# Kernel optimization log

Measured on AMD Instinct MI355X. Metric: run time of the kernel, lower is better.

The kernel has to match this reference:

```python
import jax, jax.numpy as jnp
import numpy as np

B, N, D, H, E, ED = 32, 256, 1024, 16, 512, 256
HD = D // H
NEG = float(np.finfo(np.float32).min)


def setup_inputs() -> dict:
    key = jax.random.key(0)
    ks = iter(jax.random.split(key, 16))
    def nrm(shape, fan_in):
        return jax.random.normal(next(ks), shape, jnp.float32) / np.sqrt(fan_in)
    return {
        "x": jax.random.normal(next(ks), (B, N, D), jnp.float32),
        "node_masks": jnp.ones((B, N), jnp.float32),
        "relation_edges": jax.random.randint(next(ks), (B, E, 2), 0, N, jnp.int64),
        "relation_masks": jnp.ones((B, E), jnp.float32),
        "relation_embeddings": jax.random.normal(next(ks), (B, E, ED), jnp.float32),
        "ln_g": jnp.ones((D,), jnp.float32), "ln_b": jnp.zeros((D,), jnp.float32),
        "Wq": nrm((D, D), D), "bq": jnp.zeros((D,), jnp.float32),
        "Wk": nrm((D, D), D), "bk": jnp.zeros((D,), jnp.float32),
        "Wv": nrm((D, D), D), "bv": jnp.zeros((D,), jnp.float32),
        "We": nrm((ED, H), ED), "be": jnp.zeros((H,), jnp.float32),
        "Wo": nrm((D, D), D), "bo": jnp.zeros((D,), jnp.float32),
        "ff_g": jnp.ones((D,), jnp.float32), "ff_b": jnp.zeros((D,), jnp.float32),
        "W1": nrm((D, 4 * D), D), "b1": jnp.zeros((4 * D,), jnp.float32),
        "W2": nrm((4 * D, D), 4 * D), "b2": jnp.zeros((D,), jnp.float32),
    }


def _ln(x, g, b):
    m = jnp.mean(x, axis=-1, keepdims=True)
    v = jnp.mean((x - m) ** 2, axis=-1, keepdims=True)
    return (x - m) / jnp.sqrt(v + 1e-5) * g + b


def reference(x, node_masks, relation_edges, relation_masks, relation_embeddings,
              ln_g, ln_b, Wq, bq, Wk, bk, Wv, bv, We, be, Wo, bo,
              ff_g, ff_b, W1, b1, W2, b2):
    residual = x
    xn = _ln(x, ln_g, ln_b)
    # [B,N,D] -> [B,H,N,HD]
    def split_heads(t):
        return t.reshape(B, N, H, HD).transpose(0, 2, 1, 3)
    q = split_heads(xn @ Wq + bq)
    k = split_heads(xn @ Wk + bk)
    v = split_heads(xn @ Wv + bv)
    attn = jnp.einsum('bhqd,bhkd->bhqk', q, k) / np.sqrt(HD)

    nb = node_masks.astype(bool)
    pair_mask = nb[:, None, :, None] & nb[:, None, None, :]  # [B,1,N,N]

    # --- scatter edge list into dense adjacency + per-head bias ---
    src = jnp.clip(relation_edges[..., 0], 0, N - 1)  # [B,E]
    dst = jnp.clip(relation_edges[..., 1], 0, N - 1)
    valid = relation_masks.astype(bool)
    # route invalid edges to a padding row/col N, sliced off afterwards
    src_w = jnp.where(valid, src, N)
    dst_w = jnp.where(valid, dst, N)
    b_idx = jnp.broadcast_to(jnp.arange(B)[:, None], (B, E))

    Np = N + 1
    adj = jnp.broadcast_to(jnp.eye(Np, dtype=bool), (B, Np, Np))
    adj = adj.at[b_idx, src_w, dst_w].set(True).at[b_idx, dst_w, src_w].set(True)
    rel_adj = adj[:, :N, :N][:, None]  # [B,1,N,N]

    eb = relation_embeddings @ We + be  # [B,E,H]
    bias = jnp.zeros((B, Np, Np, H), x.dtype)
    bias = bias.at[b_idx, src_w, dst_w].set(eb).at[b_idx, dst_w, src_w].set(eb)
    rel_bias = bias[:, :N, :N, :].transpose(0, 3, 1, 2)  # [B,H,N,N]

    attn = attn + rel_bias
    pair_mask = pair_mask & rel_adj
    attn = jnp.where(pair_mask, attn, NEG)
    attn = jax.nn.softmax(attn, axis=-1)
    attn = jnp.nan_to_num(attn)

    out = jnp.einsum('bhqk,bhkd->bhqd', attn, v).transpose(0, 2, 1, 3).reshape(B, N, D)
    x = residual + (out @ Wo + bo)
    h = _ln(x, ff_g, ff_b)
    h = jax.nn.silu(h @ W1 + b1) @ W2 + b2
    x = x + h
    return x * node_masks[..., None]
```

## Files before the change

kernel.cpp:

```cpp
#include <hip/hip_runtime.h>
#include <math.h>

#define B_  32
#define N_  256
#define D_  1024
#define H_  16
#define E_  512
#define ED_ 256
#define HD_ 64
#define QS_ 3072
#define NEG_ (-3.4028234663852886e38f)

typedef __attribute__((ext_vector_type(8))) short short8;
typedef __attribute__((ext_vector_type(4))) float f32x4;
typedef __attribute__((ext_vector_type(16))) float f32x16;
typedef unsigned short ushort_t;
typedef unsigned int uint_t;

union U16x8 { uint4 u4; ushort_t s[8]; };

static __device__ __forceinline__ ushort_t f2bf(float f) {
    uint_t u = __builtin_bit_cast(uint_t, f);
    u = (u + 0x7fff + ((u >> 16) & 1)) >> 16;
    return (ushort_t)u;
}

static __device__ __forceinline__ void gload_lds16(const void* g, void* l) {
    __builtin_amdgcn_global_load_lds(
        (const __attribute__((address_space(1))) unsigned int*)g,
        (__attribute__((address_space(3))) unsigned int*)l, 16, 0, 0);
}

__global__ __launch_bounds__(256) void ln_bf16_kernel(const float* __restrict__ x,
                                                      const float* __restrict__ g,
                                                      const float* __restrict__ b,
                                                      ushort_t* __restrict__ out) {
    int row = blockIdx.x;
    const float* xr = x + (size_t)row * D_;
    ushort_t* yr = out + (size_t)row * D_;
    __shared__ float red[256];
    int t = threadIdx.x;
    float vals[4];
    float s = 0.f;
#pragma unroll
    for (int i = 0; i < 4; ++i) { vals[i] = xr[t + i * 256]; s += vals[i]; }
    red[t] = s; __syncthreads();
    for (int off = 128; off > 0; off >>= 1) { if (t < off) red[t] += red[t + off]; __syncthreads(); }
    float mean = red[0] * (1.f / D_);
    __syncthreads();
    float vs = 0.f;
#pragma unroll
    for (int i = 0; i < 4; ++i) { float d = vals[i] - mean; vs += d * d; }
    red[t] = vs; __syncthreads();
    for (int off = 128; off > 0; off >>= 1) { if (t < off) red[t] += red[t + off]; __syncthreads(); }
    float rstd = 1.f / sqrtf(red[0] * (1.f / D_) + 1e-5f);
#pragma unroll
    for (int i = 0; i < 4; ++i) {
        int c = t + i * 256;
        yr[c] = f2bf((vals[i] - mean) * rstd * g[c] + b[c]);
    }
}

__global__ __launch_bounds__(256) void prep_kernel(
    const float* __restrict__ Wq, const float* __restrict__ Wk,
    const float* __restrict__ Wv, const float* __restrict__ Wo,
    const float* __restrict__ W1, const float* __restrict__ W2,
    const float* __restrict__ bq, const float* __restrict__ bk,
    const float* __restrict__ bv,
    ushort_t* __restrict__ qkvT, ushort_t* __restrict__ WoT,
    ushort_t* __restrict__ W1T, ushort_t* __restrict__ W2T,
    float* __restrict__ cb)
{
    int id = blockIdx.x;
    if (id >= 12288) {
        int i = (id - 12288) * 256 + threadIdx.x;
        cb[i] = (i < 1024) ? bq[i] : ((i < 2048) ? bk[i - 1024] : bv[i - 2048]);
        return;
    }
    const float* in; ushort_t* outp; int K, N, tid;
    if (id < 4096) {
        int wsel = id >> 10; tid = id & 1023; K = D_; N = D_;
        in   = (wsel == 0) ? Wq : (wsel == 1) ? Wk : (wsel == 2) ? Wv : Wo;
        outp = (wsel == 0) ? qkvT : (wsel == 1) ? qkvT + 1024 * 1024
             : (wsel == 2) ? qkvT + 2 * 1024 * 1024 : WoT;
    } else if (id < 8192) { tid = id - 4096; K = D_; N = 4 * D_; in = W1; outp = W1T; }
    else                  { tid = id - 8192; K = 4 * D_; N = D_; in = W2; outp = W2T; }
    int tilesX = N >> 5;
    int n0 = (tid % tilesX) * 32, k0 = (tid / tilesX) * 32;

    __shared__ float tile[32][33];
    int tx = threadIdx.x & 31, ty = threadIdx.x >> 5;
#pragma unroll
    for (int r = 0; r < 4; ++r)
        tile[ty + r * 8][tx] = in[(size_t)(k0 + ty + r * 8) * N + n0 + tx];
    __syncthreads();
#pragma unroll
    for (int r = 0; r < 4; ++r)
        outp[(size_t)(n0 + ty + r * 8) * K + k0 + tx] = f2bf(tile[tx][ty + r * 8]);
}

__global__ __launch_bounds__(256) void eb_kernel(const float* __restrict__ re,
                                                 const float* __restrict__ We,
                                                 const float* __restrict__ be,
                                                 float* __restrict__ eb) {
    __shared__ float rs[16 * 256];
    __shared__ float wl[256 * 16];
    int t = threadIdx.x;
    int be0 = blockIdx.x * 16;
#pragma unroll
    for (int i = 0; i < 16; ++i) wl[t + i * 256] = We[t + i * 256];
#pragma unroll
    for (int i = 0; i < 16; ++i) rs[t + i * 256] = re[(size_t)be0 * 256 + t + i * 256];
    __syncthreads();
    int el = t >> 4, h = t & 15;
    float s = be[h];
#pragma unroll 8
    for (int i = 0; i < 256; ++i) s += rs[el * 256 + i] * wl[i * 16 + h];
    eb[(size_t)(be0 + el) * 16 + h] = s;
}

__global__ void scatter_kernel(const int* __restrict__ edges, const float* __restrict__ emask,
                               int* __restrict__ prio) {
    int idx = blockIdx.x * blockDim.x + threadIdx.x;
    if (idx >= B_ * E_) return;
    if (emask[idx] == 0.f) return;
    int b = idx / E_, e = idx % E_;
    int s = edges[2 * idx], d = edges[2 * idx + 1];
    s = min(max(s, 0), N_ - 1);
    d = min(max(d, 0), N_ - 1);
    int* base = prio + (size_t)b * N_ * N_;
    atomicMax(&base[s * N_ + d], e);
    atomicMax(&base[d * N_ + s], e + E_);
}

template<int MODE>
__global__ __launch_bounds__(256) void gemm_bf16(
    const ushort_t* __restrict__ A, const ushort_t* __restrict__ BT,
    const float* __restrict__ bias, const float* __restrict__ res,
    const float* __restrict__ nm, void* __restrict__ Cout,
    int M, int N, int K)
{
    __shared__ ushort_t As[128 * 32];
    __shared__ ushort_t Bs[128 * 32];
    int t = threadIdx.x;
    int lane = t & 63;
    int l31 = lane & 31, lh = lane >> 5;
    int w = t >> 6;
    int wr = (w >> 1) * 64, wc = (w & 1) * 64;

    int bid = blockIdx.x;
    int xcd = bid & 7;
    int lid = bid >> 3;
    int st  = lid >> 5;
    int ls  = lid & 31;
    int brow = xcd * 8 + (ls >> 2);
    int bcol = st * 4 + (ls & 3);
    int row0 = brow * 128, col0 = bcol * 128;

    const ushort_t* Ag = A + (size_t)row0 * K;
    const ushort_t* Bg = BT + (size_t)col0 * K;
    int r0 = t >> 2;
    int sl = t & 3;
    int sc = (sl ^ ((r0 >> 1) & 3)) * 8;

    f32x16 acc[2][2];
#pragma unroll
    for (int i = 0; i < 2; ++i)
#pragma unroll
        for (int j = 0; j < 2; ++j)
#pragma unroll
            for (int r = 0; r < 16; ++r) acc[i][j][r] = 0.f;

    for (int k0 = 0; k0 < K; k0 += 32) {
        gload_lds16(Ag + (size_t)r0 * K + k0 + sc, (char*)As + t * 16);
        gload_lds16(Ag + (size_t)(64 + r0) * K + k0 + sc, (char*)As + 4096 + t * 16);
        gload_lds16(Bg + (size_t)r0 * K + k0 + sc, (char*)Bs + t * 16);
        gload_lds16(Bg + (size_t)(64 + r0) * K + k0 + sc, (char*)Bs + 4096 + t * 16);
        __syncthreads();
#pragma unroll
        for (int ks = 0; ks < 2; ++ks) {
            short8 af[2], bf[2];
#pragma unroll
            for (int it = 0; it < 2; ++it) {
                int m = wr + it * 32 + l31;
                int x = ((ks * 2 + lh) ^ ((m >> 1) & 3)) * 8;
                af[it] = *(const short8*)(const void*)(As + m * 32 + x);
            }
#pragma unroll
            for (int jt = 0; jt < 2; ++jt) {
                int n = wc + jt * 32 + l31;
                int x = ((ks * 2 + lh) ^ ((n >> 1) & 3)) * 8;
                bf[jt] = *(const short8*)(const void*)(Bs + n * 32 + x);
            }
#pragma unroll
            for (int it = 0; it < 2; ++it)
#pragma unroll
                for (int jt = 0; jt < 2; ++jt)
                    acc[it][jt] = __builtin_amdgcn_mfma_f32_32x32x16_bf16(af[it], bf[jt], acc[it][jt], 0, 0, 0);
        }
        __syncthreads();
    }

#pragma unroll
    for (int it = 0; it < 2; ++it) {
#pragma unroll
        for (int jt = 0; jt < 2; ++jt) {
            int col = col0 + wc + jt * 32 + l31;
            float bcol_b = bias[col];
#pragma unroll
            for (int reg = 0; reg < 16; ++reg) {
                int row = row0 + wr + it * 32 + (reg & 3) + 8 * (reg >> 2) + 4 * lh;
                float v = acc[it][jt][reg] + bcol_b;
                if (MODE == 0) {
                    ((ushort_t*)Cout)[(size_t)row * N + col] = f2bf(v);
                } else if (MODE == 1) {
                    ((float*)Cout)[(size_t)row * N + col] = v + res[(size_t)row * N + col];
                } else if (MODE == 2) {
                    v = v / (1.f + __expf(-v));
                    ((ushort_t*)Cout)[(size_t)row * N + col] = f2bf(v);
                } else {
                    v = (v + res[(size_t)row * N + col]) * nm[row];
                    ((float*)Cout)[(size_t)row * N + col] = v;
                }
            }
        }
    }
}

__global__ __launch_bounds__(256, 2) void attn_mfma_kernel(
    const ushort_t* __restrict__ qkv, const int* __restrict__ prio,
    const float* __restrict__ eb, const float* __restrict__ nm,
    ushort_t* __restrict__ out)
{
    int xb = blockIdx.x;
    int bid = (xb & 7) * 256 + (xb >> 3);
    int h = bid & 15, qt = (bid >> 4) & 3, b = bid >> 6;
    int t = threadIdx.x;

    __shared__ ushort_t Ks[256 * 72];
    __shared__ ushort_t Vt[64 * 264];

    int lane = t & 63, c = lane & 15, quad = lane >> 4;
    int w = t >> 6;
    int qbase = qt * 64 + w * 16 + quad * 4;

    int pr[16][4];
    const int* prp = prio + ((size_t)(b * N_ + qbase)) * N_ + c;
#pragma unroll
    for (int j = 0; j < 16; ++j)
#pragma unroll
        for (int r = 0; r < 4; ++r)
            pr[j][r] = prp[(size_t)r * N_ + j * 16];

    float nmq[4];
#pragma unroll
    for (int r = 0; r < 4; ++r) nmq[r] = nm[b * N_ + qbase + r];
    float nmk[16];
#pragma unroll
    for (int j = 0; j < 16; ++j) nmk[j] = nm[b * N_ + j * 16 + c];

    const ushort_t* qg = qkv + ((size_t)(b * N_ + qt * 64 + w * 16 + c)) * QS_ + h * HD_;
    short8 aq0 = *(const short8*)(const void*)(qg + quad * 8);
    short8 aq1 = *(const short8*)(const void*)(qg + 32 + quad * 8);

    int lr = t >> 3, lc = (t & 7) * 8;
    const ushort_t* kg = qkv + ((size_t)(b * N_)) * QS_ + 1024 + h * HD_;
#pragma unroll
    for (int r = 0; r < 256; r += 32)
        *(uint4*)&Ks[(lr + r) * 72 + lc] = *(const uint4*)&kg[(size_t)(lr + r) * QS_ + lc];
    const ushort_t* vg = qkv + ((size_t)(b * N_)) * QS_ + 2048 + h * HD_;
#pragma unroll
    for (int r = 0; r < 256; r += 32) {
        U16x8 uu; uu.u4 = *(const uint4*)&vg[(size_t)(lr + r) * QS_ + lc];
#pragma unroll
        for (int i = 0; i < 8; ++i)
            Vt[(lc + i) * 264 + lr + r] = uu.s[i];
    }

    const float* ebb = eb + (size_t)b * E_ * H_ + h;
    float badd[16][4];
#pragma unroll
    for (int j = 0; j < 16; ++j) {
        int key = j * 16 + c;
#pragma unroll
        for (int r = 0; r < 4; ++r) {
            int p = pr[j][r];
            float bias = 0.f;
            bool adj = (key == qbase + r);
            if (p >= 0) {
                int e = (p >= E_) ? p - E_ : p;
                bias = ebb[(size_t)e * H_];
                adj = true;
            }
            bool ok = adj && (nmq[r] != 0.f) && (nmk[j] != 0.f);
            badd[j][r] = ok ? bias : -3.0e38f;
        }
    }
    __syncthreads();

    f32x4 z = {0.f, 0.f, 0.f, 0.f};
    f32x4 acc[16];
#pragma unroll
    for (int j = 0; j < 16; ++j) acc[j] = z;
    __builtin_amdgcn_s_setprio(1);
#pragma unroll
    for (int j = 0; j < 16; ++j) {
        short8 b0 = *(const short8*)(const void*)(Ks + (j * 16 + c) * 72 + quad * 8);
        short8 b1 = *(const short8*)(const void*)(Ks + (j * 16 + c) * 72 + 32 + quad * 8);
        acc[j] = __builtin_amdgcn_mfma_f32_16x16x32_bf16(aq0, b0, acc[j], 0, 0, 0);
        acc[j] = __builtin_amdgcn_mfma_f32_16x16x32_bf16(aq1, b1, acc[j], 0, 0, 0);
    }
    __builtin_amdgcn_s_setprio(0);

#pragma unroll
    for (int j = 0; j < 16; ++j)
#pragma unroll
        for (int r = 0; r < 4; ++r)
            acc[j][r] = acc[j][r] * 0.125f + badd[j][r];

    float inv[4];
#pragma unroll
    for (int r = 0; r < 4; ++r) {
        float m = acc[0][r];
#pragma unroll
        for (int j = 1; j < 16; ++j) m = fmaxf(m, acc[j][r]);
        m = fmaxf(m, __shfl_xor(m, 1));
        m = fmaxf(m, __shfl_xor(m, 2));
        m = fmaxf(m, __shfl_xor(m, 4));
        m = fmaxf(m, __shfl_xor(m, 8));
        float s = 0.f;
#pragma unroll
        for (int j = 0; j < 16; ++j) {
            float p = __expf(acc[j][r] - m);
            acc[j][r] = p;
            s += p;
        }
        s += __shfl_xor(s, 1);
        s += __shfl_xor(s, 2);
        s += __shfl_xor(s, 4);
        s += __shfl_xor(s, 8);
        inv[r] = 1.f / s;
    }

    __syncthreads();
    ushort_t* Ps = Ks;
#pragma unroll
    for (int j = 0; j < 16; ++j)
#pragma unroll
        for (int r = 0; r < 4; ++r)
            Ps[(w * 16 + quad * 4 + r) * 264 + j * 16 + c] = f2bf(acc[j][r] * inv[r]);
    asm volatile("s_waitcnt lgkmcnt(0)" ::: "memory");

    f32x4 oc[4];
#pragma unroll
    for (int dt = 0; dt < 4; ++dt) oc[dt] = z;
    __builtin_amdgcn_s_setprio(1);
#pragma unroll
    for (int k0 = 0; k0 < 256; k0 += 32) {
        short8 ap = *(const short8*)(const void*)(Ps + (w * 16 + c) * 264 + k0 + quad * 8);
#pragma unroll
        for (int dt = 0; dt < 4; ++dt) {
            short8 bv = *(const short8*)(const void*)(Vt + (dt * 16 + c) * 264 + k0 + quad * 8);
            oc[dt] = __builtin_amdgcn_mfma_f32_16x16x32_bf16(ap, bv, oc[dt], 0, 0, 0);
        }
    }
    __builtin_amdgcn_s_setprio(0);
    ushort_t* og = out + ((size_t)(b * N_ + qt * 64 + w * 16)) * D_ + h * HD_;
#pragma unroll
    for (int dt = 0; dt < 4; ++dt)
#pragma unroll
        for (int r = 0; r < 4; ++r)
            og[(size_t)(quad * 4 + r) * D_ + dt * 16 + c] = f2bf(oc[dt][r]);
}

extern "C" void kernel_launch(void* const* d_in, const int* in_sizes, int n_in,
                              void* d_out, int out_size, void* d_ws, size_t ws_size,
                              hipStream_t stream) {
    const float* x     = (const float*)d_in[0];
    const float* nm    = (const float*)d_in[1];
    const int*   edges = (const int*)d_in[2];
    const float* emask = (const float*)d_in[3];
    const float* remb  = (const float*)d_in[4];
    const float* ln_g  = (const float*)d_in[5];
    const float* ln_b  = (const float*)d_in[6];
    const float* Wq = (const float*)d_in[7];  const float* bq = (const float*)d_in[8];
    const float* Wk = (const float*)d_in[9];  const float* bk = (const float*)d_in[10];
    const float* Wv = (const float*)d_in[11]; const float* bv = (const float*)d_in[12];
    const float* We = (const float*)d_in[13]; const float* be = (const float*)d_in[14];
    const float* Wo = (const float*)d_in[15]; const float* bo = (const float*)d_in[16];
    const float* ff_g = (const float*)d_in[17]; const float* ff_b = (const float*)d_in[18];
    const float* W1 = (const float*)d_in[19]; const float* b1 = (const float*)d_in[20];
    const float* W2 = (const float*)d_in[21]; const float* b2 = (const float*)d_in[22];
    float* out = (float*)d_out;

    char* ws = (char*)d_ws;
    const size_t MB = 1ll << 20;
    int*      prio = (int*)ws;
    float*    ebuf = (float*)(ws + 8 * MB);
    ushort_t* xn   = (ushort_t*)(ws + 9 * MB);
    float*    x2   = (float*)(ws + 25 * MB);
    ushort_t* hn   = (ushort_t*)(ws + 57 * MB);
    ushort_t* qkv  = (ushort_t*)(ws + 73 * MB);
    ushort_t* mid  = qkv;
    ushort_t* qkvT = (ushort_t*)(ws + 137 * MB);
    ushort_t* WoT  = (ushort_t*)(ws + 143 * MB);
    ushort_t* W1T  = (ushort_t*)(ws + 145 * MB);
    ushort_t* W2T  = (ushort_t*)(ws + 153 * MB);
    float*    cb   = (float*)(ws + 161 * MB);
    ushort_t* aout = xn;

    const int M = B_ * N_;

    (void)hipMemsetAsync(prio, 0xFF, (size_t)B_ * N_ * N_ * sizeof(int), stream);
    eb_kernel<<<B_ * E_ / 16, 256, 0, stream>>>(remb, We, be, ebuf);
    scatter_kernel<<<(B_ * E_ + 255) / 256, 256, 0, stream>>>(edges, emask, prio);

    prep_kernel<<<12300, 256, 0, stream>>>(Wq, Wk, Wv, Wo, W1, W2, bq, bk, bv,
                                           qkvT, WoT, W1T, W2T, cb);

    ln_bf16_kernel<<<M, 256, 0, stream>>>(x, ln_g, ln_b, xn);

    gemm_bf16<0><<<24 * 64, 256, 0, stream>>>(xn, qkvT, cb, nullptr, nullptr, qkv, M, QS_, D_);

    attn_mfma_kernel<<<B_ * H_ * 4, 256, 0, stream>>>(qkv, prio, ebuf, nm, aout);

    gemm_bf16<1><<<8 * 64, 256, 0, stream>>>(aout, WoT, bo, x, nullptr, x2, M, D_, D_);
    ln_bf16_kernel<<<M, 256, 0, stream>>>(x2, ff_g, ff_b, hn);

    gemm_bf16<2><<<32 * 64, 256, 0, stream>>>(hn, W1T, b1, nullptr, nullptr, mid, M, 4 * D_, D_);
    gemm_bf16<3><<<8 * 64, 256, 0, stream>>>(mid, W2T, b2, x2, nm, out, M, D_, 4 * D_);
}
```

Before: 524.5 us.

## Add 256x256-tile double-buffered MFMA GEMM for QKV and FFN-up projections

```diff
diff --git a/kernel.cpp b/kernel.cpp
--- a/kernel.cpp
+++ b/kernel.cpp
@@ -211,13 +211,8 @@
             for (int reg = 0; reg < 16; ++reg) {
                 int row = row0 + wr + it * 32 + (reg & 3) + 8 * (reg >> 2) + 4 * lh;
                 float v = acc[it][jt][reg] + bcol_b;
-                if (MODE == 0) {
-                    ((ushort_t*)Cout)[(size_t)row * N + col] = f2bf(v);
-                } else if (MODE == 1) {
+                if (MODE == 1) {
                     ((float*)Cout)[(size_t)row * N + col] = v + res[(size_t)row * N + col];
-                } else if (MODE == 2) {
-                    v = v / (1.f + __expf(-v));
-                    ((ushort_t*)Cout)[(size_t)row * N + col] = f2bf(v);
                 } else {
                     v = (v + res[(size_t)row * N + col]) * nm[row];
                     ((float*)Cout)[(size_t)row * N + col] = v;
@@ -225,6 +220,126 @@
             }
         }
     }
+}
+
+template<int MODE, int NBN>
+__global__ __launch_bounds__(512) void gemm256(
+    const ushort_t* __restrict__ A, const ushort_t* __restrict__ BT,
+    const float* __restrict__ bias, void* __restrict__ Cout,
+    int M, int N, int K)
+{
+    __shared__ ushort_t Asm_[2][2][128 * 64];
+    __shared__ ushort_t Bsm_[2][2][128 * 64];
+
+    int t = threadIdx.x;
+    int lane = t & 63;
+    int w = t >> 6;
+    int wm = w >> 2, wn = w & 3;
+    int c2 = lane & 15, quad = lane >> 4;
+
+    int bid = blockIdx.x;
+    int xcd = bid & 7, lid = bid >> 3;
+    int brow = xcd * 4 + lid / NBN;
+    int bcol = lid % NBN;
+    int row0 = brow * 256, col0 = bcol * 256;
+
+    const ushort_t* Ag = A + (size_t)row0 * K;
+    const ushort_t* Bg = BT + (size_t)col0 * K;
+
+    int srow = t >> 3, slot = t & 7;
+    int schunk8 = (slot ^ (srow & 7)) * 8;
+
+    auto stage_half = [&](int bf, int hh, int kt) {
+        const ushort_t* g = (hh < 2) ? Ag : Bg;
+        int h = hh & 1;
+        char* l = (hh < 2) ? (char*)&Asm_[bf][h][0] : (char*)&Bsm_[bf][h][0];
+        gload_lds16(g + (size_t)(h * 128 + srow) * K + kt * 64 + schunk8, l + t * 16);
+        gload_lds16(g + (size_t)(h * 128 + 64 + srow) * K + kt * 64 + schunk8, l + 8192 + t * 16);
+    };
+
+    int choff[2];
+    choff[0] = ((0 * 4 + quad) ^ (c2 & 7)) * 16;
+    choff[1] = ((1 * 4 + quad) ^ (c2 & 7)) * 16;
+    const int bhalf = wn >> 1;
+    const int bco = (wn & 1) * 64;
+
+    f32x4 acc[8][4];
+#pragma unroll
+    for (int a_ = 0; a_ < 8; ++a_)
+#pragma unroll
+        for (int b_ = 0; b_ < 4; ++b_)
+#pragma unroll
+            for (int r = 0; r < 4; ++r) acc[a_][b_][r] = 0.f;
+
+    stage_half(0, 0, 0); stage_half(0, 1, 0); stage_half(0, 2, 0); stage_half(0, 3, 0);
+
+    int T = K >> 6;
+    for (int i = 0; i < (T >> 1); ++i) {
+#pragma unroll
+        for (int hf = 0; hf < 2; ++hf) {
+            int tau = 2 * i + hf;
+            int bufc = tau & 1;
+            short8 bfr[4][2];
+#pragma unroll
+            for (int q = 0; q < 4; ++q) {
+                if (tau + 1 < T) stage_half((tau + 1) & 1, q, tau + 1);
+                if (q == 0) {
+                    if (tau + 1 < T) asm volatile("s_waitcnt vmcnt(2)" ::: "memory");
+                    else             asm volatile("s_waitcnt vmcnt(0)" ::: "memory");
+                }
+                __builtin_amdgcn_s_barrier();
+                __builtin_amdgcn_sched_barrier(0);
+                if (q == 0) {
+#pragma unroll
+                    for (int jt = 0; jt < 4; ++jt)
+#pragma unroll
+                        for (int ks = 0; ks < 2; ++ks)
+                            bfr[jt][ks] = *(const short8*)((const char*)&Bsm_[bufc][bhalf][0]
+                                           + (bco + jt * 16 + c2) * 128 + choff[ks]);
+                }
+                short8 afr[2][2];
+#pragma unroll
+                for (int it = 0; it < 2; ++it)
+#pragma unroll
+                    for (int ks = 0; ks < 2; ++ks)
+                        afr[it][ks] = *(const short8*)((const char*)&Asm_[bufc][wm][0]
+                                       + (q * 32 + it * 16 + c2) * 128 + choff[ks]);
+                asm volatile("s_waitcnt lgkmcnt(0)" ::: "memory");
+                __builtin_amdgcn_sched_barrier(0);
+                __builtin_amdgcn_s_setprio(1);
+#pragma unroll
+                for (int it = 0; it < 2; ++it)
+#pragma unroll
+                    for (int jt = 0; jt < 4; ++jt) {
+                        acc[q * 2 + it][jt] = __builtin_amdgcn_mfma_f32_16x16x32_bf16(
+                            afr[it][0], bfr[jt][0], acc[q * 2 + it][jt], 0, 0, 0);
+                        acc[q * 2 + it][jt] = __builtin_amdgcn_mfma_f32_16x16x32_bf16(
+                            afr[it][1], bfr[jt][1], acc[q * 2 + it][jt], 0, 0, 0);
+                    }
+                __builtin_amdgcn_s_setprio(0);
+                __builtin_amdgcn_sched_barrier(0);
+                __builtin_amdgcn_s_barrier();
+            }
+        }
+    }
+
+#pragma unroll
+    for (int q = 0; q < 4; ++q)
+#pragma unroll
+        for (int it = 0; it < 2; ++it) {
+            int row = row0 + wm * 128 + q * 32 + it * 16 + quad * 4;
+#pragma unroll
+            for (int jt = 0; jt < 4; ++jt) {
+                int col = col0 + wn * 64 + jt * 16 + c2;
+                float bc = bias[col];
+#pragma unroll
+                for (int r = 0; r < 4; ++r) {
+                    float v = acc[q * 2 + it][jt][r] + bc;
+                    if (MODE == 2) v = v / (1.f + __expf(-v));
+                    ((ushort_t*)Cout)[(size_t)(row + r) * N + col] = f2bf(v);
+                }
+            }
+        }
 }
 
 __global__ __launch_bounds__(256, 2) void attn_mfma_kernel(
@@ -420,13 +535,13 @@
 
     ln_bf16_kernel<<<M, 256, 0, stream>>>(x, ln_g, ln_b, xn);
 
-    gemm_bf16<0><<<24 * 64, 256, 0, stream>>>(xn, qkvT, cb, nullptr, nullptr, qkv, M, QS_, D_);
+    gemm256<0, 12><<<384, 512, 0, stream>>>(xn, qkvT, cb, qkv, M, QS_, D_);
 
     attn_mfma_kernel<<<B_ * H_ * 4, 256, 0, stream>>>(qkv, prio, ebuf, nm, aout);
 
     gemm_bf16<1><<<8 * 64, 256, 0, stream>>>(aout, WoT, bo, x, nullptr, x2, M, D_, D_);
     ln_bf16_kernel<<<M, 256, 0, stream>>>(x2, ff_g, ff_b, hn);
 
-    gemm_bf16<2><<<32 * 64, 256, 0, stream>>>(hn, W1T, b1, nullptr, nullptr, mid, M, 4 * D_, D_);
+    gemm256<2, 16><<<512, 512, 0, stream>>>(hn, W1T, b1, mid, M, 4 * D_, D_);
     gemm_bf16<3><<<8 * 64, 256, 0, stream>>>(mid, W2T, b2, x2, nm, out, M, D_, 4 * D_);
 }
```

After: 536.4 us. 2.3% more time.
